# Performance work log

Hardware: AMD Instinct MI355X
Metric: run time of the kernel (lower is better)

The kernel has to match this reference:

```python
import jax, jax.numpy as jnp
import numpy as np

# dims: Q queries, K hops (topk), N relation groups, M padded nodes/group
Q, K, N, M = 64, 2, 32, 64
E, D, R, S = 256, 1024, 200, 8192  # embs_size, model_size, n_rel, seq positions


def setup_inputs() -> dict:
    key = jax.random.key(0)
    ks = jax.random.split(key, 10)
    hidden_states = jax.random.normal(ks[0], (S, D), jnp.float32)
    nodes = jax.random.normal(ks[1], (Q, K, N, M, E), jnp.float32)
    # ragged groups: zero-pad beyond a random valid length (mirrors F.pad + stack)
    lengths = jax.random.randint(ks[2], (Q, K, N), 1, M + 1)
    valid = jnp.arange(M)[None, None, None, :] < lengths[..., None]
    nodes = nodes * valid[..., None]
    prob_idx = jax.random.randint(ks[3], (Q, K, N), 0, R)
    gnn_idx = jnp.arange(Q, dtype=jnp.int32)          # gnn_mask positions
    rel_idx = jnp.arange(Q, dtype=jnp.int32) + Q      # rel_mask positions (disjoint)
    sc = lambda fan: float(1.0 / np.sqrt(fan))
    u = lambda k, shp, fan: jax.random.uniform(k, shp, jnp.float32, -sc(fan), sc(fan))
    Wc = u(ks[4], (D, R), D); bc = jnp.zeros((R,), jnp.float32)
    Wq = u(ks[5], (D, D), D); bq = jnp.zeros((D,), jnp.float32)
    Wn = u(ks[6], (E, D), E); bn = jnp.zeros((D,), jnp.float32)
    Wg = u(ks[7], (E, D), E); bg = jnp.zeros((D,), jnp.float32)
    return {"hidden_states": hidden_states, "nodes": nodes, "prob_idx": prob_idx,
            "gnn_idx": gnn_idx, "rel_idx": rel_idx,
            "Wc": Wc, "bc": bc, "Wq": Wq, "bq": bq,
            "Wn": Wn, "bn": bn, "Wg": Wg, "bg": bg}


def reference(hidden_states, nodes, prob_idx, gnn_idx, rel_idx,
              Wc, bc, Wq, bq, Wn, bn, Wg, bg):
    Qn, Kn, Nn, Mn, En = nodes.shape
    # classification_head: Linear + Softmax over relations
    rel_prob = jax.nn.softmax(hidden_states[rel_idx] @ Wc + bc, axis=1)  # [Q,R]
    # gather per-group relation probabilities (extract_values_from_tensor)
    probs = jnp.take_along_axis(rel_prob, prob_idx.reshape(Qn, Kn * Nn), axis=1)
    probs = probs.reshape(Qn, Kn, Nn)                                     # [Q,K,N]
    # mask from first feature of padded node embeddings (as in calculate_scores)
    mask = nodes[..., 0] != 0                                             # [Q,K,N,M]
    # query_reprj and nodes_reprj (Linear + Tanh)
    gq = jnp.tanh(hidden_states[gnn_idx] @ Wq + bq)                       # [Q,D]
    gn = jnp.tanh(jnp.einsum('qknme,ed->qknmd', nodes, Wn) + bn)          # [Q,K,N,M,D]
    dots = jnp.einsum('qknmd,qd->qknm', gn, gq)                           # [Q,K,N,M]
    attn = jax.nn.softmax(dots, axis=3)            # softmax over nodes within group
    logits = attn * probs[..., None] / 0.1         # scale by group prob / temperature
    # global softmax over all (group, node) slots per (query, hop)
    wa = jax.nn.softmax(logits.reshape(Qn, Kn, Nn * Mn), axis=-1)
    wa = wa.reshape(Qn, Kn, Nn, Mn)
    wa = jnp.where(mask, wa, 0.0)
    # weighted mean over the flattened N*M slots, then mean over topk hops
    mean_emb = jnp.mean(nodes * wa[..., None], axis=(2, 3))               # [Q,K,E]
    pooled = mean_emb.mean(axis=1)                                        # [Q,E]
    out = jnp.tanh(pooled @ Wg + bg)                                      # gnn_reprj
    return hidden_states.at[gnn_idx].add(out)
```

## Files before the change

### kernel.cpp

```cpp
#include <hip/hip_runtime.h>
#include <hip/hip_bf16.h>
#include <math.h>

#define QDIM 64
#define KDIM 2
#define NDIM 32
#define MDIM 64
#define EDIM 256
#define DDIM 1024
#define RDIM 200
#define SDIM 8192
#define GCOUNT (QDIM * KDIM * NDIM)

typedef short short8_t __attribute__((ext_vector_type(8)));
typedef float f32x4 __attribute__((ext_vector_type(4)));

__device__ __forceinline__ float tanh_c(float x) {
    float e = __expf(2.0f * x);
    return 1.0f - 2.0f * __builtin_amdgcn_rcpf(1.0f + e);
}

__device__ __forceinline__ uint32_t f2bf(float f) {
    uint32_t u = __float_as_uint(f);
    return (u + 0x7fffu + ((u >> 16) & 1u)) >> 16;
}
__device__ __forceinline__ float bf2f(unsigned short h) {
    return __uint_as_float(((uint32_t)h) << 16);
}

__global__ __launch_bounds__(256) void prologue_kernel(
    const float* __restrict__ hs, float* __restrict__ out,
    const float* __restrict__ Wn, short* __restrict__ wnpk,
    const int* __restrict__ gnn_idx, const float* __restrict__ Wq,
    const float* __restrict__ bq, float* __restrict__ gqo,
    const int* __restrict__ rel_idx, const float* __restrict__ Wc,
    const float* __restrict__ bc, float* __restrict__ rel_prob,
    const float* __restrict__ nodes, int* __restrict__ nvarr) {
    const int b = blockIdx.x, t = threadIdx.x;
    __shared__ float row[DDIM];
    __shared__ float arr[256];

    if (b < 2048) {
        const float4* src = (const float4*)hs;
        float4* dst = (float4*)out;
        int i = b * 256 + t;
#pragma unroll
        for (int r = 0; r < 4; ++r) dst[i + r * 524288] = src[i + r * 524288];
    } else if (b < 2176) {
        int tid = (b - 2048) * 256 + t;
        int lane = tid & 63, ks = (tid >> 6) & 7, ntg = tid >> 9;
        int low = lane & 15, hi = lane >> 4;
        short8_t o;
#pragma unroll
        for (int j = 0; j < 8; ++j) {
            int k = ks * 32 + hi * 8 + j;
            int d = ntg * 16 + low;
            o[j] = (short)f2bf(Wn[(size_t)k * DDIM + d]);
        }
        *(short8_t*)(wnpk + (size_t)tid * 8) = o;
    } else if (b < 2432) {
        int bb = b - 2176;
        int q = bb >> 2, seg = bb & 3;
        const float* src = hs + (size_t)gnn_idx[q] * DDIM;
        for (int i = t; i < DDIM; i += 256) row[i] = src[i];
        __syncthreads();
        int d = seg * 256 + t;
        float a = bq[d];
#pragma unroll 8
        for (int k = 0; k < DDIM; ++k) a += row[k] * Wq[(size_t)k * DDIM + d];
        gqo[(size_t)q * DDIM + d] = tanh_c(a);
    } else if (b < 2496) {
        int q = b - 2432;
        const float* src = hs + (size_t)rel_idx[q] * DDIM;
        for (int i = t; i < DDIM; i += 256) row[i] = src[i];
        __syncthreads();
        float lg = -INFINITY;
        if (t < RDIM) {
            float a = bc[t];
            for (int k = 0; k < DDIM; ++k) a += row[k] * Wc[(size_t)k * RDIM + t];
            lg = a;
        }
        arr[t] = lg;
        __syncthreads();
        for (int s = 128; s > 0; s >>= 1) {
            if (t < s) arr[t] = fmaxf(arr[t], arr[t + s]);
            __syncthreads();
        }
        float mx = arr[0];
        __syncthreads();
        float ex = (t < RDIM) ? __expf(lg - mx) : 0.0f;
        arr[t] = ex;
        __syncthreads();
        for (int s = 128; s > 0; s >>= 1) {
            if (t < s) arr[t] += arr[t + s];
            __syncthreads();
        }
        float sm = arr[0];
        if (t < RDIM) rel_prob[q * RDIM + t] = ex / sm;
    } else {
        int g = (b - 2496) * 4 + (t >> 6);
        int lane = t & 63;
        float f0 = nodes[(size_t)g * (MDIM * EDIM) + (size_t)lane * EDIM];
        unsigned long long mk = __ballot(f0 != 0.0f);
        if (lane == 0) nvarr[g] = __popcll(mk);
    }
}

__global__ __launch_bounds__(64) void pack_jobs(const int* __restrict__ nvarr,
                                                const float* __restrict__ bn,
                                                const float* __restrict__ gq,
                                                int4* __restrict__ glist4,
                                                float* __restrict__ cqarr) {
    int q = blockIdx.x, t = threadIdx.x;
    __shared__ int lists[4][64];
    __shared__ int cnt[4];
    float cp = 0.f;
#pragma unroll
    for (int i = 0; i < 16; ++i) {
        int d = i * 64 + t;
        cp += tanh_c(bn[d]) * gq[(size_t)q * DDIM + d];
    }
#pragma unroll
    for (int off = 32; off > 0; off >>= 1) cp += __shfl_xor(cp, off);
    if (t == 0) cqarr[q] = cp;

    if (t < 4) cnt[t] = 0;
    __syncthreads();
    int g = q * 64 + t;
    int nv = nvarr[g];
    int mt = (nv + 15) >> 4;
    if (mt < 1) mt = 1;
    if (mt > 4) mt = 4;
    int pos = atomicAdd(&cnt[mt - 1], 1);
    lists[mt - 1][pos] = g;
    __syncthreads();
    if (t == 0) {
        int c1 = cnt[0], c2 = cnt[1], c3 = cnt[2], c4 = cnt[3];
        int i1 = 0, i2 = 0, i3 = 0, i4 = 0, j = 0;
        int4* outp = glist4 + q * 64;
        const int D = GCOUNT;
        while (i4 < c4) outp[j++] = make_int4(lists[3][i4++] | (0 << 20), D, D, D);
        while (i3 < c3) {
            int g1 = (i1 < c1) ? lists[0][i1++] : D;
            outp[j++] = make_int4(lists[2][i3++] | (1 << 20), g1, D, D);
        }
        while (i2 + 1 < c2) {
            int a = lists[1][i2++], b2 = lists[1][i2++];
            outp[j++] = make_int4(a | (2 << 20), b2, D, D);
        }
        if (i2 < c2) {
            int a = lists[1][i2++];
            int b2 = (i1 < c1) ? lists[0][i1++] : D;
            int c = (i1 < c1) ? lists[0][i1++] : D;
            outp[j++] = make_int4(a | (3 << 20), b2, c, D);
        }
        while (i1 < c1) {
            int a = lists[0][i1++];
            int b2 = (i1 < c1) ? lists[0][i1++] : D;
            int c = (i1 < c1) ? lists[0][i1++] : D;
            int d2 = (i1 < c1) ? lists[0][i1++] : D;
            outp[j++] = make_int4(a | (4 << 20), b2, c, d2);
        }
        while (j < 64) outp[j++] = make_int4(-1, -1, -1, -1);
    }
}

#define STEP2(CUR, NXT, NTG)                                                               \
    {                                                                                      \
        int pn_ = (NTG) + 1;                                                               \
        pn_ = pn_ > 63 ? 63 : pn_;                                                         \
        const short8_t* pp_ = bbase + (size_t)pn_ * 512;                                   \
        _Pragma("unroll") for (int ks = 0; ks < 8; ++ks) NXT[ks] = pp_[ks * 64];           \
        float2 pv_ = pairs[(NTG)*16 + low];                                                \
        f32x4 a0 = {0.f, 0.f, 0.f, 0.f}, a1 = a0;                                          \
        _Pragma("unroll") for (int ks = 0; ks < 8; ++ks) {                                 \
            a0 = __builtin_amdgcn_mfma_f32_16x16x32_bf16(af[0][ks], CUR[ks], a0, 0, 0, 0); \
            a1 = __builtin_amdgcn_mfma_f32_16x16x32_bf16(af[1][ks], CUR[ks], a1, 0, 0, 0); \
        }                                                                                  \
        float bnv_ = pv_.x, gqv_ = pv_.y;                                                  \
        _Pragma("unroll") for (int jj = 0; jj < 4; ++jj) {                                 \
            dacc[0][jj] += tanh_c(a0[jj] + bnv_) * gqv_;                                   \
            dacc[1][jj] += tanh_c(a1[jj] + bnv_) * gqv_;                                   \
        }                                                                                  \
    }

__global__ __launch_bounds__(256, 3) void phase1_mfma(
    const float* __restrict__ nodes, const short* __restrict__ wnpk,
    const float* __restrict__ bn, const float* __restrict__ gq,
    const float* __restrict__ rel_prob, const int* __restrict__ prob_idx,
    const int4* __restrict__ glist4, const float* __restrict__ cqarr,
    float* __restrict__ gvec, float* __restrict__ gden, float* __restrict__ gmx) {
    __shared__ alignas(16) char transit[4][8192];
    __shared__ float2 pairs[DDIM];
    __shared__ float vecu[8][EDIM];
    __shared__ float dots_s[128];
    __shared__ float lv_s[128];
    __shared__ float mk_s[128];

    const int tid = threadIdx.x;
    const int w = tid >> 6, lane = tid & 63;
    const int low = lane & 15, hi = lane >> 4;

    const int4 jb0 = glist4[2 * blockIdx.x];
    const int4 jb1 = glist4[2 * blockIdx.x + 1];
    if (jb0.x < 0 && jb1.x < 0) return;
    const int4 jb = (w < 2) ? jb0 : jb1;
    const bool live = jb.x >= 0;
    const int q = ((jb0.x >= 0 ? jb0.x : jb1.x) & 0xFFFF) >> 6;
    const float cqv = cqarr[q];

    const unsigned tabs[5] = {0x30201000u, 0x01201000u, 0x11011000u, 0x02011000u,
                              0x03020100u};
    const int gA[4] = {jb.x & 0xFFFF, jb.y, jb.z, jb.w};
    const unsigned tb = live ? tabs[(jb.x >> 20) & 7] : 0;

    int usrc[2] = {GCOUNT, GCOUNT};
    short8_t af[2][8];
    if (live) {
        char* ldsw = transit[w];
#pragma unroll
        for (int u2 = 0; u2 < 2; ++u2) {
            int u = (w & 1) * 2 + u2;
            int byte_ = (tb >> (u * 8)) & 0xFF;
            int slot = byte_ & 0xF, tile = byte_ >> 4;
            int gs = gA[slot];
            usrc[u2] = gs;
            int lg = (gs >= GCOUNT) ? 0 : gs;
            const float4* src =
                (const float4*)(nodes + ((size_t)lg * MDIM + tile * 16) * EDIM);
#pragma unroll
            for (int i = 0; i < 16; ++i) {
                int idx4 = i * 64 + lane;
                float4 v = src[idx4];
                int r = idx4 >> 6, c4 = idx4 & 63;
                int off = (r * 512 + c4 * 8) ^ ((r & 7) << 4);
                uint32_t w0 = f2bf(v.x) | (f2bf(v.y) << 16);
                uint32_t w1 = f2bf(v.z) | (f2bf(v.w) << 16);
                *(uint2*)(ldsw + off) = make_uint2(w0, w1);
            }
            asm volatile("s_waitcnt lgkmcnt(0)" ::: "memory");
#pragma unroll
            for (int ks = 0; ks < 8; ++ks) {
                int off = (low * 512 + ks * 64 + hi * 16) ^ ((low & 7) << 4);
                af[u2][ks] = *(const short8_t*)(ldsw + off);
            }
            asm volatile("s_waitcnt lgkmcnt(0)" ::: "memory");
        }
    }

    {
        const float* gqrow = gq + (size_t)q * DDIM;
#pragma unroll
        for (int i = 0; i < 4; ++i) {
            int d = tid + i * 256;
            pairs[d] = make_float2(bn[d], gqrow[d]);
        }
    }
    __syncthreads();

    float dacc[2][4] = {};
    if (live) {
        const short8_t* bbase = (const short8_t*)wnpk + lane;
        short8_t bA[8], bB[8];
#pragma unroll
        for (int ks = 0; ks < 8; ++ks) bA[ks] = bbase[ks * 64];
        for (int it = 0; it < 32; ++it) {
            STEP2(bA, bB, 2 * it);
            STEP2(bB, bA, 2 * it + 1);
        }
#pragma unroll
        for (int u2 = 0; u2 < 2; ++u2)
#pragma unroll
            for (int jj = 0; jj < 4; ++jj) {
                float v = dacc[u2][jj];
                v += __shfl_xor(v, 1);
                v += __shfl_xor(v, 2);
                v += __shfl_xor(v, 4);
                v += __shfl_xor(v, 8);
                dacc[u2][jj] = v;
            }
        if (low == 0) {
#pragma unroll
            for (int u2 = 0; u2 < 2; ++u2)
#pragma unroll
                for (int jj = 0; jj < 4; ++jj)
                    dots_s[(w * 2 + u2) * 16 + hi * 4 + jj] = dacc[u2][jj];
        }
        if (hi == 0) {
#pragma unroll
            for (int u2 = 0; u2 < 2; ++u2) {
                unsigned short s0 = (unsigned short)af[u2][0][0];
                mk_s[(w * 2 + u2) * 16 + low] = ((s0 & 0x7fffu) != 0) ? 1.0f : 0.0f;
            }
        }
    }
    __syncthreads();

    const int NGT[5] = {1, 2, 2, 3, 4};
    const int U0T[5][4] = {{0, 0, 0, 0}, {0, 3, 0, 0}, {0, 2, 0, 0},
                           {0, 2, 3, 0}, {0, 1, 2, 3}};
    const int NUT[5][4] = {{4, 0, 0, 0}, {3, 1, 0, 0}, {2, 2, 0, 0},
                           {2, 1, 1, 0}, {1, 1, 1, 1}};
    const int ng0 = (jb0.x >= 0) ? NGT[(jb0.x >> 20) & 7] : 0;
    const int ng1 = (jb1.x >= 0) ? NGT[(jb1.x >> 20) & 7] : 0;
    const int ngtot = ng0 + ng1;

    for (int gi = w; gi < ngtot; gi += 4) {
        int jx = (gi < ng0) ? 0 : 1;
        int4 J = jx ? jb1 : jb0;
        int li = jx ? gi - ng0 : gi;
        int shp = (J.x >> 20) & 7;
        int U0 = U0T[shp][li] + jx * 4;
        int NU = NUT[shp][li];
        int gg = (li == 0) ? (J.x & 0xFFFF) : (li == 1) ? J.y : (li == 2) ? J.z : J.w;
        if (gg >= GCOUNT) continue;
        int NS = NU * 16, TL = 64 - NS;
        float dv = (lane < NS) ? dots_s[U0 * 16 + lane] : -INFINITY;
        float mx = dv;
#pragma unroll
        for (int o = 32; o > 0; o >>= 1) mx = fmaxf(mx, __shfl_xor(mx, o));
        if (TL > 0) mx = fmaxf(mx, cqv);
        float ex = (lane < NS) ? __expf(dv - mx) : 0.f;
        float sm = ex;
#pragma unroll
        for (int o = 32; o > 0; o >>= 1) sm += __shfl_xor(sm, o);
        float ext = __expf(cqv - mx);
        if (TL > 0) sm += (float)TL * ext;
        float pr = rel_prob[(size_t)q * RDIM + prob_idx[gg]];
        float p10 = pr * 10.0f / sm;
        float l2 = ex * p10;
        float lgvt = ext * p10;
        float gm = (lane < NS) ? l2 : -INFINITY;
#pragma unroll
        for (int o = 32; o > 0; o >>= 1) gm = fmaxf(gm, __shfl_xor(gm, o));
        if (TL > 0) gm = fmaxf(gm, lgvt);
        float el = (lane < NS) ? __expf(l2 - gm) : 0.f;
        float den = el;
#pragma unroll
        for (int o = 32; o > 0; o >>= 1) den += __shfl_xor(den, o);
        if (TL > 0) den += (float)TL * __expf(lgvt - gm);
        if (lane < NS) lv_s[U0 * 16 + lane] = el * mk_s[U0 * 16 + lane];
        if (lane == 0) {
            gden[gg] = den;
            gmx[gg] = gm;
        }
    }
    __syncthreads();

    if (live) {
#pragma unroll
        for (int u2 = 0; u2 < 2; ++u2) {
            if (usrc[u2] >= GCOUNT) continue;
            int ug = w * 2 + u2;
            float lvm = lv_s[ug * 16 + low];
#pragma unroll
            for (int ks = 0; ks < 8; ++ks) {
                float acj[8];
#pragma unroll
                for (int j = 0; j < 8; ++j)
                    acj[j] = bf2f((unsigned short)af[u2][ks][j]) * lvm;
#pragma unroll
                for (int j = 0; j < 8; ++j) {
                    float a = acj[j];
                    a += __shfl_xor(a, 1);
                    a += __shfl_xor(a, 2);
                    a += __shfl_xor(a, 4);
                    a += __shfl_xor(a, 8);
                    acj[j] = a;
                }
                if (low == 0) {
#pragma unroll
                    for (int j = 0; j < 8; ++j) vecu[ug][ks * 32 + hi * 8 + j] = acj[j];
                }
            }
        }
    }
    __syncthreads();

    for (int gi = w; gi < ngtot; gi += 4) {
        int jx = (gi < ng0) ? 0 : 1;
        int4 J = jx ? jb1 : jb0;
        int li = jx ? gi - ng0 : gi;
        int shp = (J.x >> 20) & 7;
        int U0 = U0T[shp][li] + jx * 4;
        int NU = NUT[shp][li];
        int gg = (li == 0) ? (J.x & 0xFFFF) : (li == 1) ? J.y : (li == 2) ? J.z : J.w;
        if (gg >= GCOUNT) continue;
#pragma unroll 4
        for (int c = 0; c < 4; ++c) {
            int e = c * 64 + lane;
            float s = 0.f;
            for (int uu = 0; uu < NU; ++uu) s += vecu[U0 + uu][e];
            gvec[(size_t)gg * EDIM + e] = s;
        }
    }
}

__global__ __launch_bounds__(256) void combine_kernel(const float* __restrict__ gvec,
                                                      const float* __restrict__ gden,
                                                      const float* __restrict__ gmx,
                                                      float* __restrict__ memb) {
    int qk = blockIdx.x, t = threadIdx.x;
    __shared__ float sgm[NDIM], sden[NDIM];
    if (t < NDIM) {
        sgm[t] = gmx[qk * NDIM + t];
        sden[t] = gden[qk * NDIM + t];
    }
    __syncthreads();
    float gm = -INFINITY;
    for (int n = 0; n < NDIM; ++n) gm = fmaxf(gm, sgm[n]);
    float gs = 0.f;
    for (int n = 0; n < NDIM; ++n) gs += sden[n] * __expf(sgm[n] - gm);
    float me = 0.f;
    for (int n = 0; n < NDIM; ++n)
        me += gvec[(size_t)(qk * NDIM + n) * EDIM + t] * __expf(sgm[n] - gm);
    memb[(size_t)qk * EDIM + t] = me / (gs * (float)(NDIM * MDIM));
}

__global__ __launch_bounds__(256) void out_kernel(const float* __restrict__ memb,
                                                  const float* __restrict__ Wg,
                                                  const float* __restrict__ bg,
                                                  const int* __restrict__ gnn_idx,
                                                  float* __restrict__ out) {
    int q = blockIdx.x, t = threadIdx.x;
    __shared__ float pooled[EDIM];
    pooled[t] = 0.5f * (memb[(size_t)(q * 2 + 0) * EDIM + t] + memb[(size_t)(q * 2 + 1) * EDIM + t]);
    __syncthreads();
    float4 a = ((const float4*)bg)[t];
    const float4* Wg4 = (const float4*)Wg;
    for (int e = 0; e < EDIM; ++e) {
        float p = pooled[e];
        float4 w = Wg4[(size_t)e * (DDIM / 4) + t];
        a.x += p * w.x; a.y += p * w.y; a.z += p * w.z; a.w += p * w.w;
    }
    float4* op = (float4*)(out + (size_t)gnn_idx[q] * DDIM);
    float4 cur = op[t];
    cur.x += tanh_c(a.x);
    cur.y += tanh_c(a.y);
    cur.z += tanh_c(a.z);
    cur.w += tanh_c(a.w);
    op[t] = cur;
}

extern "C" void kernel_launch(void* const* d_in, const int* in_sizes, int n_in,
                              void* d_out, int out_size, void* d_ws, size_t ws_size,
                              hipStream_t stream) {
    const float* hs = (const float*)d_in[0];
    const float* nodes = (const float*)d_in[1];
    const int* prob_idx = (const int*)d_in[2];
    const int* gnn_idx = (const int*)d_in[3];
    const int* rel_idx = (const int*)d_in[4];
    const float* Wc = (const float*)d_in[5];
    const float* bc = (const float*)d_in[6];
    const float* Wq = (const float*)d_in[7];
    const float* bq = (const float*)d_in[8];
    const float* Wn = (const float*)d_in[9];
    const float* bn = (const float*)d_in[10];
    const float* Wg = (const float*)d_in[11];
    const float* bg = (const float*)d_in[12];
    float* out = (float*)d_out;
    float* ws = (float*)d_ws;

    float* relprob = ws;
    float* gqbuf = ws + 16384;
    float* gvec = gqbuf + 65536;
    float* gdenA = gvec + 1048832;
    float* gmaxA = gdenA + 4352;
    float* membuf = gmaxA + 4352;
    short* wnpk = (short*)(membuf + 32768);
    int* nvarr = (int*)(ws + 1303296);
    int4* glist4 = (int4*)(ws + 1307392);
    float* cqarr = ws + 1323776;

    prologue_kernel<<<3520, 256, 0, stream>>>(hs, out, Wn, wnpk, gnn_idx, Wq, bq,
                                              gqbuf, rel_idx, Wc, bc, relprob,
                                              nodes, nvarr);
    pack_jobs<<<QDIM, 64, 0, stream>>>(nvarr, bn, gqbuf, glist4, cqarr);
    phase1_mfma<<<GCOUNT / 2, 256, 0, stream>>>(nodes, wnpk, bn, gqbuf, relprob,
                                                prob_idx, glist4, cqarr, gvec, gdenA,
                                                gmaxA);
    combine_kernel<<<QDIM * KDIM, 256, 0, stream>>>(gvec, gdenA, gmaxA, membuf);
    out_kernel<<<QDIM, 256, 0, stream>>>(membuf, Wg, bg, gnn_idx, out);
}
```

Before: 263.9 us.

## Give each block one job with one 16-row tile per wave, split K across accumulators

```diff
diff --git a/kernel.cpp b/kernel.cpp
--- a/kernel.cpp
+++ b/kernel.cpp
@@ -165,22 +165,21 @@
     }
 }
 
-#define STEP2(CUR, NXT, NTG)                                                               \
+#define STEP1(CUR, NXT, NTG)                                                               \
     {                                                                                      \
         int pn_ = (NTG) + 1;                                                               \
         pn_ = pn_ > 63 ? 63 : pn_;                                                         \
         const short8_t* pp_ = bbase + (size_t)pn_ * 512;                                   \
         _Pragma("unroll") for (int ks = 0; ks < 8; ++ks) NXT[ks] = pp_[ks * 64];           \
         float2 pv_ = pairs[(NTG)*16 + low];                                                \
-        f32x4 a0 = {0.f, 0.f, 0.f, 0.f}, a1 = a0;                                          \
-        _Pragma("unroll") for (int ks = 0; ks < 8; ++ks) {                                 \
-            a0 = __builtin_amdgcn_mfma_f32_16x16x32_bf16(af[0][ks], CUR[ks], a0, 0, 0, 0); \
-            a1 = __builtin_amdgcn_mfma_f32_16x16x32_bf16(af[1][ks], CUR[ks], a1, 0, 0, 0); \
+        f32x4 aA = {0.f, 0.f, 0.f, 0.f}, aB = aA;                                          \
+        _Pragma("unroll") for (int ks = 0; ks < 4; ++ks) {                                 \
+            aA = __builtin_amdgcn_mfma_f32_16x16x32_bf16(af[ks], CUR[ks], aA, 0, 0, 0);    \
+            aB = __builtin_amdgcn_mfma_f32_16x16x32_bf16(af[ks + 4], CUR[ks + 4], aB, 0, 0, 0); \
         }                                                                                  \
         float bnv_ = pv_.x, gqv_ = pv_.y;                                                  \
         _Pragma("unroll") for (int jj = 0; jj < 4; ++jj) {                                 \
-            dacc[0][jj] += tanh_c(a0[jj] + bnv_) * gqv_;                                   \
-            dacc[1][jj] += tanh_c(a1[jj] + bnv_) * gqv_;                                   \
+            dacc[jj] += tanh_c(aA[jj] + aB[jj] + bnv_) * gqv_;                             \
         }                                                                                  \
     }
 
@@ -190,61 +189,44 @@
     const float* __restrict__ rel_prob, const int* __restrict__ prob_idx,
     const int4* __restrict__ glist4, const float* __restrict__ cqarr,
     float* __restrict__ gvec, float* __restrict__ gden, float* __restrict__ gmx) {
-    __shared__ alignas(16) char transit[4][8192];
     __shared__ float2 pairs[DDIM];
-    __shared__ float vecu[8][EDIM];
-    __shared__ float dots_s[128];
-    __shared__ float lv_s[128];
-    __shared__ float mk_s[128];
+    __shared__ float vecu[4][EDIM];
+    __shared__ float dots_s[64];
+    __shared__ float lv_s[64];
+    __shared__ float mk_s[64];
 
     const int tid = threadIdx.x;
     const int w = tid >> 6, lane = tid & 63;
     const int low = lane & 15, hi = lane >> 4;
 
-    const int4 jb0 = glist4[2 * blockIdx.x];
-    const int4 jb1 = glist4[2 * blockIdx.x + 1];
-    if (jb0.x < 0 && jb1.x < 0) return;
-    const int4 jb = (w < 2) ? jb0 : jb1;
-    const bool live = jb.x >= 0;
-    const int q = ((jb0.x >= 0 ? jb0.x : jb1.x) & 0xFFFF) >> 6;
+    const int4 jb = glist4[blockIdx.x];
+    if (jb.x < 0) return;
+    const int shape = (jb.x >> 20) & 7;
+    const int gA[4] = {jb.x & 0xFFFF, jb.y, jb.z, jb.w};
+    const int q = gA[0] >> 6;
     const float cqv = cqarr[q];
 
     const unsigned tabs[5] = {0x30201000u, 0x01201000u, 0x11011000u, 0x02011000u,
                               0x03020100u};
-    const int gA[4] = {jb.x & 0xFFFF, jb.y, jb.z, jb.w};
-    const unsigned tb = live ? tabs[(jb.x >> 20) & 7] : 0;
-
-    int usrc[2] = {GCOUNT, GCOUNT};
-    short8_t af[2][8];
-    if (live) {
-        char* ldsw = transit[w];
-#pragma unroll
-        for (int u2 = 0; u2 < 2; ++u2) {
-            int u = (w & 1) * 2 + u2;
-            int byte_ = (tb >> (u * 8)) & 0xFF;
-            int slot = byte_ & 0xF, tile = byte_ >> 4;
-            int gs = gA[slot];
-            usrc[u2] = gs;
-            int lg = (gs >= GCOUNT) ? 0 : gs;
-            const float4* src =
-                (const float4*)(nodes + ((size_t)lg * MDIM + tile * 16) * EDIM);
-#pragma unroll
-            for (int i = 0; i < 16; ++i) {
-                int idx4 = i * 64 + lane;
-                float4 v = src[idx4];
-                int r = idx4 >> 6, c4 = idx4 & 63;
-                int off = (r * 512 + c4 * 8) ^ ((r & 7) << 4);
-                uint32_t w0 = f2bf(v.x) | (f2bf(v.y) << 16);
-                uint32_t w1 = f2bf(v.z) | (f2bf(v.w) << 16);
-                *(uint2*)(ldsw + off) = make_uint2(w0, w1);
-            }
-            asm volatile("s_waitcnt lgkmcnt(0)" ::: "memory");
-#pragma unroll
-            for (int ks = 0; ks < 8; ++ks) {
-                int off = (low * 512 + ks * 64 + hi * 16) ^ ((low & 7) << 4);
-                af[u2][ks] = *(const short8_t*)(ldsw + off);
-            }
-            asm volatile("s_waitcnt lgkmcnt(0)" ::: "memory");
+    const int byte_ = (tabs[shape] >> (w * 8)) & 0xFF;
+    const int slot = byte_ & 0xF, tile = byte_ >> 4;
+    const int usrc = gA[slot];
+    const int lg = (usrc >= GCOUNT) ? 0 : usrc;
+
+    short8_t af[8];
+    {
+        const float* rowp =
+            nodes + ((size_t)lg * MDIM + tile * 16 + low) * EDIM + hi * 8;
+#pragma unroll
+        for (int ks = 0; ks < 8; ++ks) {
+            float4 a = *(const float4*)(rowp + ks * 32);
+            float4 b = *(const float4*)(rowp + ks * 32 + 4);
+            short8_t o;
+            o[0] = (short)f2bf(a.x); o[1] = (short)f2bf(a.y);
+            o[2] = (short)f2bf(a.z); o[3] = (short)f2bf(a.w);
+            o[4] = (short)f2bf(b.x); o[5] = (short)f2bf(b.y);
+            o[6] = (short)f2bf(b.z); o[7] = (short)f2bf(b.w);
+            af[ks] = o;
         }
     }
 
@@ -258,41 +240,33 @@
     }
     __syncthreads();
 
-    float dacc[2][4] = {};
-    if (live) {
+    float dacc[4] = {};
+    {
         const short8_t* bbase = (const short8_t*)wnpk + lane;
         short8_t bA[8], bB[8];
 #pragma unroll
         for (int ks = 0; ks < 8; ++ks) bA[ks] = bbase[ks * 64];
         for (int it = 0; it < 32; ++it) {
-            STEP2(bA, bB, 2 * it);
-            STEP2(bB, bA, 2 * it + 1);
-        }
-#pragma unroll
-        for (int u2 = 0; u2 < 2; ++u2)
-#pragma unroll
-            for (int jj = 0; jj < 4; ++jj) {
-                float v = dacc[u2][jj];
-                v += __shfl_xor(v, 1);
-                v += __shfl_xor(v, 2);
-                v += __shfl_xor(v, 4);
-                v += __shfl_xor(v, 8);
-                dacc[u2][jj] = v;
-            }
-        if (low == 0) {
-#pragma unroll
-            for (int u2 = 0; u2 < 2; ++u2)
-#pragma unroll
-                for (int jj = 0; jj < 4; ++jj)
-                    dots_s[(w * 2 + u2) * 16 + hi * 4 + jj] = dacc[u2][jj];
-        }
-        if (hi == 0) {
-#pragma unroll
-            for (int u2 = 0; u2 < 2; ++u2) {
-                unsigned short s0 = (unsigned short)af[u2][0][0];
-                mk_s[(w * 2 + u2) * 16 + low] = ((s0 & 0x7fffu) != 0) ? 1.0f : 0.0f;
-            }
-        }
+            STEP1(bA, bB, 2 * it);
+            STEP1(bB, bA, 2 * it + 1);
+        }
+    }
+#pragma unroll
+    for (int jj = 0; jj < 4; ++jj) {
+        float v = dacc[jj];
+        v += __shfl_xor(v, 1);
+        v += __shfl_xor(v, 2);
+        v += __shfl_xor(v, 4);
+        v += __shfl_xor(v, 8);
+        dacc[jj] = v;
+    }
+    if (low == 0) {
+#pragma unroll
+        for (int jj = 0; jj < 4; ++jj) dots_s[w * 16 + hi * 4 + jj] = dacc[jj];
+    }
+    if (hi == 0) {
+        unsigned short s0 = (unsigned short)af[0][0];
+        mk_s[w * 16 + low] = ((s0 & 0x7fffu) != 0) ? 1.0f : 0.0f;
     }
     __syncthreads();
 
@@ -301,18 +275,12 @@
                            {0, 2, 3, 0}, {0, 1, 2, 3}};
     const int NUT[5][4] = {{4, 0, 0, 0}, {3, 1, 0, 0}, {2, 2, 0, 0},
                            {2, 1, 1, 0}, {1, 1, 1, 1}};
-    const int ng0 = (jb0.x >= 0) ? NGT[(jb0.x >> 20) & 7] : 0;
-    const int ng1 = (jb1.x >= 0) ? NGT[(jb1.x >> 20) & 7] : 0;
-    const int ngtot = ng0 + ng1;
-
-    for (int gi = w; gi < ngtot; gi += 4) {
-        int jx = (gi < ng0) ? 0 : 1;
-        int4 J = jx ? jb1 : jb0;
-        int li = jx ? gi - ng0 : gi;
-        int shp = (J.x >> 20) & 7;
-        int U0 = U0T[shp][li] + jx * 4;
-        int NU = NUT[shp][li];
-        int gg = (li == 0) ? (J.x & 0xFFFF) : (li == 1) ? J.y : (li == 2) ? J.z : J.w;
+    const int ng = NGT[shape];
+
+    for (int gi = w; gi < ng; gi += 4) {
+        int U0 = U0T[shape][gi];
+        int NU = NUT[shape][gi];
+        int gg = gA[gi];
         if (gg >= GCOUNT) continue;
         int NS = NU * 16, TL = 64 - NS;
         float dv = (lane < NS) ? dots_s[U0 * 16 + lane] : -INFINITY;
@@ -347,44 +315,34 @@
     }
     __syncthreads();
 
-    if (live) {
-#pragma unroll
-        for (int u2 = 0; u2 < 2; ++u2) {
-            if (usrc[u2] >= GCOUNT) continue;
-            int ug = w * 2 + u2;
-            float lvm = lv_s[ug * 16 + low];
-#pragma unroll
-            for (int ks = 0; ks < 8; ++ks) {
-                float acj[8];
-#pragma unroll
-                for (int j = 0; j < 8; ++j)
-                    acj[j] = bf2f((unsigned short)af[u2][ks][j]) * lvm;
-#pragma unroll
-                for (int j = 0; j < 8; ++j) {
-                    float a = acj[j];
-                    a += __shfl_xor(a, 1);
-                    a += __shfl_xor(a, 2);
-                    a += __shfl_xor(a, 4);
-                    a += __shfl_xor(a, 8);
-                    acj[j] = a;
-                }
-                if (low == 0) {
-#pragma unroll
-                    for (int j = 0; j < 8; ++j) vecu[ug][ks * 32 + hi * 8 + j] = acj[j];
-                }
+    if (usrc < GCOUNT) {
+        float lvm = lv_s[w * 16 + low];
+#pragma unroll
+        for (int ks = 0; ks < 8; ++ks) {
+            float acj[8];
+#pragma unroll
+            for (int j = 0; j < 8; ++j) acj[j] = bf2f((unsigned short)af[ks][j]) * lvm;
+#pragma unroll
+            for (int j = 0; j < 8; ++j) {
+                float a = acj[j];
+                a += __shfl_xor(a, 1);
+                a += __shfl_xor(a, 2);
+                a += __shfl_xor(a, 4);
+                a += __shfl_xor(a, 8);
+                acj[j] = a;
             }
-        }
-    }
-    __syncthreads();
-
-    for (int gi = w; gi < ngtot; gi += 4) {
-        int jx = (gi < ng0) ? 0 : 1;
-        int4 J = jx ? jb1 : jb0;
-        int li = jx ? gi - ng0 : gi;
-        int shp = (J.x >> 20) & 7;
-        int U0 = U0T[shp][li] + jx * 4;
-        int NU = NUT[shp][li];
-        int gg = (li == 0) ? (J.x & 0xFFFF) : (li == 1) ? J.y : (li == 2) ? J.z : J.w;
+            if (low == 0) {
+#pragma unroll
+                for (int j = 0; j < 8; ++j) vecu[w][ks * 32 + hi * 8 + j] = acj[j];
+            }
+        }
+    }
+    __syncthreads();
+
+    for (int gi = w; gi < ng; gi += 4) {
+        int U0 = U0T[shape][gi];
+        int NU = NUT[shape][gi];
+        int gg = gA[gi];
         if (gg >= GCOUNT) continue;
 #pragma unroll 4
         for (int c = 0; c < 4; ++c) {
@@ -476,9 +434,9 @@
                                               gqbuf, rel_idx, Wc, bc, relprob,
                                               nodes, nvarr);
     pack_jobs<<<QDIM, 64, 0, stream>>>(nvarr, bn, gqbuf, glist4, cqarr);
-    phase1_mfma<<<GCOUNT / 2, 256, 0, stream>>>(nodes, wnpk, bn, gqbuf, relprob,
-                                                prob_idx, glist4, cqarr, gvec, gdenA,
-                                                gmaxA);
+    phase1_mfma<<<QDIM * 64, 256, 0, stream>>>(nodes, wnpk, bn, gqbuf, relprob,
+                                               prob_idx, glist4, cqarr, gvec, gdenA,
+                                               gmaxA);
     combine_kernel<<<QDIM * KDIM, 256, 0, stream>>>(gvec, gdenA, gmaxA, membuf);
     out_kernel<<<QDIM, 256, 0, stream>>>(membuf, Wg, bg, gnn_idx, out);
 }
```

New measurement: 413.2 us. 1.57x slower.

## Stage Wn tiles through LDS with async global_load_lds double buffering

Applied to the files above, without the earlier changes.

```diff
diff --git a/kernel.cpp b/kernel.cpp
--- a/kernel.cpp
+++ b/kernel.cpp
@@ -11,6 +11,9 @@
 #define RDIM 200
 #define SDIM 8192
 #define GCOUNT (QDIM * KDIM * NDIM)
+
+#define GLOBAL_AS __attribute__((address_space(1)))
+#define LDS_AS __attribute__((address_space(3)))
 
 typedef short short8_t __attribute__((ext_vector_type(8)));
 typedef float f32x4 __attribute__((ext_vector_type(4)));
@@ -165,37 +168,18 @@
     }
 }
 
-#define STEP2(CUR, NXT, NTG)                                                               \
-    {                                                                                      \
-        int pn_ = (NTG) + 1;                                                               \
-        pn_ = pn_ > 63 ? 63 : pn_;                                                         \
-        const short8_t* pp_ = bbase + (size_t)pn_ * 512;                                   \
-        _Pragma("unroll") for (int ks = 0; ks < 8; ++ks) NXT[ks] = pp_[ks * 64];           \
-        float2 pv_ = pairs[(NTG)*16 + low];                                                \
-        f32x4 a0 = {0.f, 0.f, 0.f, 0.f}, a1 = a0;                                          \
-        _Pragma("unroll") for (int ks = 0; ks < 8; ++ks) {                                 \
-            a0 = __builtin_amdgcn_mfma_f32_16x16x32_bf16(af[0][ks], CUR[ks], a0, 0, 0, 0); \
-            a1 = __builtin_amdgcn_mfma_f32_16x16x32_bf16(af[1][ks], CUR[ks], a1, 0, 0, 0); \
-        }                                                                                  \
-        float bnv_ = pv_.x, gqv_ = pv_.y;                                                  \
-        _Pragma("unroll") for (int jj = 0; jj < 4; ++jj) {                                 \
-            dacc[0][jj] += tanh_c(a0[jj] + bnv_) * gqv_;                                   \
-            dacc[1][jj] += tanh_c(a1[jj] + bnv_) * gqv_;                                   \
-        }                                                                                  \
-    }
-
 __global__ __launch_bounds__(256, 3) void phase1_mfma(
     const float* __restrict__ nodes, const short* __restrict__ wnpk,
     const float* __restrict__ bn, const float* __restrict__ gq,
     const float* __restrict__ rel_prob, const int* __restrict__ prob_idx,
     const int4* __restrict__ glist4, const float* __restrict__ cqarr,
     float* __restrict__ gvec, float* __restrict__ gden, float* __restrict__ gmx) {
-    __shared__ alignas(16) char transit[4][8192];
-    __shared__ float2 pairs[DDIM];
-    __shared__ float vecu[8][EDIM];
-    __shared__ float dots_s[128];
-    __shared__ float lv_s[128];
-    __shared__ float mk_s[128];
+    __shared__ alignas(16) char lds[34304];
+    float2* pairs = (float2*)(lds + 16384);
+    float(*vecu)[EDIM] = (float(*)[EDIM])(lds + 24576);
+    float* dots_s = (float*)(lds + 32768);
+    float* lv_s = dots_s + 128;
+    float* mk_s = lv_s + 128;
 
     const int tid = threadIdx.x;
     const int w = tid >> 6, lane = tid & 63;
@@ -217,7 +201,7 @@
     int usrc[2] = {GCOUNT, GCOUNT};
     short8_t af[2][8];
     if (live) {
-        char* ldsw = transit[w];
+        char* ldsw = lds + w * 8192;
 #pragma unroll
         for (int u2 = 0; u2 < 2; ++u2) {
             int u = (w & 1) * 2 + u2;
@@ -247,6 +231,7 @@
             asm volatile("s_waitcnt lgkmcnt(0)" ::: "memory");
         }
     }
+    __syncthreads();
 
     {
         const float* gqrow = gq + (size_t)q * DDIM;
@@ -256,18 +241,48 @@
             pairs[d] = make_float2(bn[d], gqrow[d]);
         }
     }
+#define STAGE_B(NT, BUF)                                                            \
+    {                                                                               \
+        const short* sb_ = wnpk + (size_t)(NT)*4096;                                \
+        _Pragma("unroll") for (int c_ = 0; c_ < 2; ++c_) {                          \
+            int seg_ = (w * 2 + c_) * 512;                              \
+            __builtin_amdgcn_global_load_lds(                                       \
+                (const GLOBAL_AS void*)(sb_ + seg_ + lane * 8),                     \
+                (LDS_AS void*)(lds + (BUF)*8192 + seg_ * 2), 16, 0, 0);             \
+        }                                                                           \
+    }
+    STAGE_B(0, 0);
+    asm volatile("s_waitcnt vmcnt(0)" ::: "memory");
     __syncthreads();
 
     float dacc[2][4] = {};
+    for (int it = 0; it < 64; ++it) {
+        const int cur = it & 1;
+        if (it < 63) STAGE_B(it + 1, cur ^ 1);
+        if (live) {
+            const short8_t* bp = (const short8_t*)(lds + cur * 8192) + lane;
+            short8_t bf[8];
+#pragma unroll
+            for (int ks = 0; ks < 8; ++ks) bf[ks] = bp[ks * 64];
+            float2 pv = pairs[it * 16 + low];
+            f32x4 a0 = {0.f, 0.f, 0.f, 0.f}, a1 = a0;
+#pragma unroll
+            for (int ks = 0; ks < 8; ++ks) {
+                a0 = __builtin_amdgcn_mfma_f32_16x16x32_bf16(af[0][ks], bf[ks], a0, 0, 0, 0);
+                a1 = __builtin_amdgcn_mfma_f32_16x16x32_bf16(af[1][ks], bf[ks], a1, 0, 0, 0);
+            }
+            float bnv = pv.x, gqv = pv.y;
+#pragma unroll
+            for (int jj = 0; jj < 4; ++jj) {
+                dacc[0][jj] += tanh_c(a0[jj] + bnv) * gqv;
+                dacc[1][jj] += tanh_c(a1[jj] + bnv) * gqv;
+            }
+        }
+        asm volatile("s_waitcnt vmcnt(0)" ::: "memory");
+        __syncthreads();
+    }
+
     if (live) {
-        const short8_t* bbase = (const short8_t*)wnpk + lane;
-        short8_t bA[8], bB[8];
-#pragma unroll
-        for (int ks = 0; ks < 8; ++ks) bA[ks] = bbase[ks * 64];
-        for (int it = 0; it < 32; ++it) {
-            STEP2(bA, bB, 2 * it);
-            STEP2(bB, bA, 2 * it + 1);
-        }
 #pragma unroll
         for (int u2 = 0; u2 < 2; ++u2)
 #pragma unroll
```

New measurement: 269.0 us. Within noise of the previous version (+1.9%).
